# Optimization experiments

Hardware: AMD Instinct MI355X
Metric: run time of the kernel (lower is better)

Reference implementation:

```python
import jax, jax.numpy as jnp
import numpy as np

B, L = 2, 1024
D_MODEL, N_LAYER, VOCAB = 768, 4, 32000
D_INNER, D_STATE, D_CONV = 2 * D_MODEL, 16, 4
DT_RANK = (D_MODEL + 15) // 16  # 48


def setup_inputs() -> dict:
    key = jax.random.key(0)
    ks = jax.random.split(key, 8)
    s = 0.02
    nl = N_LAYER
    A_init = jnp.tile(jnp.log(jnp.arange(1.0, D_STATE + 1.0, dtype=jnp.float32))[None, None, :], (nl, D_INNER, 1))
    return {
        "sequence": jax.random.randint(ks[0], (B, L), 0, VOCAB),
        "sequence_mask": jnp.ones((B, L), dtype=jnp.int32),
        "emb": jax.random.normal(ks[1], (VOCAB, D_MODEL)) * s,
        "norm_w": jnp.ones((nl, D_MODEL)),
        "in_proj_w": jax.random.normal(ks[2], (nl, 2 * D_INNER, D_MODEL)) * s,
        "conv_w": jax.random.normal(ks[3], (nl, D_INNER, D_CONV)) * s,
        "conv_b": jnp.zeros((nl, D_INNER)),
        "x_proj_w": jax.random.normal(ks[4], (nl, DT_RANK + 2 * D_STATE, D_INNER)) * s,
        "dt_w": jax.random.normal(ks[5], (nl, D_INNER, DT_RANK)) * s,
        "dt_b": jnp.log(jnp.expm1(jnp.full((nl, D_INNER), 1e-2))),  # inv-softplus(dt_init)
        "A_log": A_init,
        "D_skip": jnp.ones((nl, D_INNER)),
        "out_w": jax.random.normal(ks[6], (nl, D_MODEL, D_INNER)) * s,
        "normf_w": jnp.ones((D_MODEL,)),
    }


def _rmsnorm(x, w, eps=1e-5):
    x = x.astype(jnp.float32)
    return x * jax.lax.rsqrt(jnp.mean(x * x, axis=-1, keepdims=True) + eps) * w


def _mamba_block(h, in_w, cw, cb, xpw, dtw, dtb, a_log, d_skip, ow):
    # h: [B, L, D_MODEL]
    Bsz, Lsz, _ = h.shape
    xz = jnp.einsum('bld,ed->ble', h, in_w)  # [B, L, 2*d_inner]
    x, z = jnp.split(xz, 2, axis=-1)
    # causal depthwise conv1d, kernel D_CONV
    xp = jnp.pad(x, ((0, 0), (D_CONV - 1, 0), (0, 0)))
    x = sum(xp[:, k:k + Lsz, :] * cw[:, k] for k in range(D_CONV)) + cb
    x = jax.nn.silu(x)
    xdbl = jnp.einsum('bld,ed->ble', x, xpw)  # [B, L, dt_rank + 2*d_state]
    dt = xdbl[..., :DT_RANK]
    Bm = xdbl[..., DT_RANK:DT_RANK + D_STATE]
    Cm = xdbl[..., DT_RANK + D_STATE:]
    delta = jax.nn.softplus(jnp.einsum('blr,dr->bld', dt, dtw) + dtb)  # [B, L, d_inner]
    A = -jnp.exp(a_log)  # [d_inner, d_state]

    def step(hstate, inp):
        d_t, b_t, c_t, u_t = inp  # [B,di],[B,ds],[B,ds],[B,di]
        dA = jnp.exp(d_t[..., None] * A)  # [B, di, ds]
        hstate = dA * hstate + (d_t * u_t)[..., None] * b_t[:, None, :]
        y = jnp.einsum('bds,bs->bd', hstate, c_t)
        return hstate, y

    h0 = jnp.zeros((Bsz, D_INNER, D_STATE), dtype=x.dtype)
    _, ys = jax.lax.scan(
        step, h0,
        (delta.transpose(1, 0, 2), Bm.transpose(1, 0, 2), Cm.transpose(1, 0, 2), x.transpose(1, 0, 2)))
    y = ys.transpose(1, 0, 2) + x * d_skip
    y = y * jax.nn.silu(z)
    return jnp.einsum('bld,ed->ble', y, ow)


def _forward(sequence, sequence_mask, emb, norm_w, in_proj_w, conv_w, conv_b,
             x_proj_w, dt_w, dt_b, A_log, D_skip, out_w, normf_w):
    residual = emb[sequence]  # [B, L, D]
    for i in range(norm_w.shape[0]):
        hn = _rmsnorm(residual, norm_w[i])
        residual = residual + _mamba_block(hn, in_proj_w[i], conv_w[i], conv_b[i],
                                           x_proj_w[i], dt_w[i], dt_b[i],
                                           A_log[i], D_skip[i], out_w[i])
    out = _rmsnorm(residual, normf_w)  # [B, L, D]
    last = sequence_mask.sum(-1).astype(jnp.int32) - 1
    return out[jnp.arange(out.shape[0]), last]  # [B, D] last valid hidden state


def reference(sequence, sequence_mask, emb, norm_w, in_proj_w, conv_w, conv_b,
              x_proj_w, dt_w, dt_b, A_log, D_skip, out_w, normf_w):
    return _forward(sequence, sequence_mask, emb, norm_w, in_proj_w, conv_w, conv_b,
                    x_proj_w, dt_w, dt_b, A_log, D_skip, out_w, normf_w)
```

## Files before the change

### kernel.cpp

```cpp
#include <hip/hip_runtime.h>
#include <hip/hip_bf16.h>

#define BSZ 2
#define LSEQ 1024
#define DMODEL 768
#define NLAYER 4
#define DINNER 1536
#define DSTATE 16
#define DCONV 4
#define DTRANK 48
#define NCHUNK 64
#define CLEN 16
#define XDSTR 128
#define XZLD (2 * DINNER)

typedef __bf16 bf16x8_t __attribute__((ext_vector_type(8)));
typedef float f32x4_t __attribute__((ext_vector_type(4)));
typedef unsigned short u16x8_t __attribute__((ext_vector_type(8)));
typedef __hip_bfloat16 bf16;

__device__ inline float bfbits2f(unsigned short u) {
    unsigned int x = ((unsigned int)u) << 16;
    return __builtin_bit_cast(float, x);
}
__device__ inline unsigned short f2bfbits(float f) {
    return __builtin_bit_cast(unsigned short, (__bf16)f);
}

__device__ __forceinline__ void gload16(const bf16* g, bf16* l) {
    __builtin_amdgcn_global_load_lds(
        (const __attribute__((address_space(1))) unsigned int*)g,
        (__attribute__((address_space(3))) unsigned int*)l,
        16, 0, 0);
}

__device__ inline float block_reduce_sum(float v, float* sbuf) {
    __syncthreads();
    #pragma unroll
    for (int o = 32; o > 0; o >>= 1) v += __shfl_down(v, o, 64);
    int wid = threadIdx.x >> 6;
    int lane = threadIdx.x & 63;
    if (lane == 0) sbuf[wid] = v;
    __syncthreads();
    if (threadIdx.x == 0) sbuf[0] = (sbuf[0] + sbuf[1]) + (sbuf[2] + sbuf[3]);
    __syncthreads();
    return sbuf[0];
}

#define PN1 (NLAYER * 3072 * 768)
#define PN2 (NLAYER * 768 * 1536)
#define PN3 (NLAYER * 128 * 1536)
#define PN4 (BSZ * LSEQ * DMODEL)
#define PN5 (2 * BSZ * LSEQ * XDSTR)
__global__ __launch_bounds__(256) void init_kernel(
    const int* __restrict__ seq, const float* __restrict__ emb,
    const float* __restrict__ in_w, const float* __restrict__ out_w,
    const float* __restrict__ xp_w,
    float* __restrict__ residual, bf16* __restrict__ in16,
    bf16* __restrict__ out16, bf16* __restrict__ xp16, float* __restrict__ xdbl2) {
    int idx = blockIdx.x * 256 + threadIdx.x;
    if (idx < PN1) { in16[idx] = __float2bfloat16(in_w[idx]); return; }
    idx -= PN1;
    if (idx < PN2) { out16[idx] = __float2bfloat16(out_w[idx]); return; }
    idx -= PN2;
    if (idx < PN3) {
        int l = idx / (128 * DINNER);
        int r = idx - l * (128 * DINNER);
        int e = r / DINNER;
        int k = r - e * DINNER;
        xp16[idx] = (e < 80) ? __float2bfloat16(xp_w[((size_t)l * 80 + e) * DINNER + k])
                             : __float2bfloat16(0.f);
        return;
    }
    idx -= PN3;
    if (idx < PN4) {
        int bl = idx / DMODEL;
        int dd = idx - bl * DMODEL;
        residual[idx] = emb[(size_t)seq[bl] * DMODEL + dd];
        return;
    }
    idx -= PN4;
    xdbl2[idx] = 0.f;
}

__global__ __launch_bounds__(256) void rmsnorm_kernel(
    const float* __restrict__ res, const float* __restrict__ w, bf16* __restrict__ out) {
    __shared__ float sbuf[8];
    int row = blockIdx.x;
    const float* x = res + (size_t)row * DMODEL;
    float ss = 0.f;
    for (int i = threadIdx.x; i < DMODEL; i += 256) { float v = x[i]; ss += v * v; }
    ss = block_reduce_sum(ss, sbuf);
    float scale = rsqrtf(ss / (float)DMODEL + 1e-5f);
    for (int i = threadIdx.x; i < DMODEL; i += 256)
        out[(size_t)row * DMODEL + i] = __float2bfloat16(x[i] * scale * w[i]);
}

__global__ __launch_bounds__(256) void rmsnorm_acc_kernel(
    float* __restrict__ res, const float* __restrict__ p0, const float* __restrict__ p1,
    const float* __restrict__ w, bf16* __restrict__ out) {
    __shared__ float sbuf[8];
    int row = blockIdx.x;
    size_t base = (size_t)row * DMODEL;
    float ss = 0.f;
    for (int i = threadIdx.x; i < DMODEL; i += 256) {
        float v = res[base + i] + p0[base + i] + p1[base + i];
        res[base + i] = v;
        ss += v * v;
    }
    ss = block_reduce_sum(ss, sbuf);
    float scale = rsqrtf(ss / (float)DMODEL + 1e-5f);
    for (int i = threadIdx.x; i < DMODEL; i += 256)
        out[base + i] = __float2bfloat16(res[base + i] * scale * w[i]);
}

__global__ __launch_bounds__(256) void gemm_128x64_g(
    const bf16* __restrict__ A, int lda, const bf16* __restrict__ Bw, int ldb,
    bf16* __restrict__ C16, int ldc, int K) {
    __shared__ bf16 As[128][64];
    __shared__ bf16 Bs[64][64];
    int tid = threadIdx.x;
    int wave = tid >> 6;
    int lane = tid & 63;
    int quad = lane >> 4;
    int l16 = lane & 15;
    int bm = blockIdx.x * 128;
    int bn = blockIdx.y * 64;
    int wm = wave * 32;
    int lr = lane >> 3;
    int lc = (lane & 7) ^ lr;
    int sx = (l16 & 7) << 3;

    f32x4_t acc[2][4];
    #pragma unroll
    for (int i = 0; i < 2; ++i)
        #pragma unroll
        for (int j = 0; j < 4; ++j) acc[i][j] = (f32x4_t){0.f, 0.f, 0.f, 0.f};

    for (int k0 = 0; k0 < K; k0 += 64) {
        #pragma unroll
        for (int i = 0; i < 6; ++i) {
            int ch = wave * 6 + i;
            if (ch < 16) {
                int r = ch * 8 + lr;
                gload16(A + (size_t)(bm + r) * lda + k0 + lc * 8, &As[ch * 8][0]);
            } else {
                int c2 = ch - 16;
                int r = c2 * 8 + lr;
                gload16(Bw + (size_t)(bn + r) * ldb + k0 + lc * 8, &Bs[c2 * 8][0]);
            }
        }
        __syncthreads();
        #pragma unroll
        for (int kk = 0; kk < 64; kk += 32) {
            bf16x8_t af[2], bf[4];
            #pragma unroll
            for (int i = 0; i < 2; ++i)
                af[i] = *(const bf16x8_t*)(&As[wm + i * 16 + l16][(kk + quad * 8) ^ sx]);
            #pragma unroll
            for (int j = 0; j < 4; ++j)
                bf[j] = *(const bf16x8_t*)(&Bs[j * 16 + l16][(kk + quad * 8) ^ sx]);
            #pragma unroll
            for (int i = 0; i < 2; ++i)
                #pragma unroll
                for (int j = 0; j < 4; ++j)
                    acc[i][j] = __builtin_amdgcn_mfma_f32_16x16x32_bf16(af[i], bf[j], acc[i][j], 0, 0, 0);
        }
        __syncthreads();
    }

    int mbase = bm + wm + quad * 4;
    #pragma unroll
    for (int i = 0; i < 2; ++i)
        #pragma unroll
        for (int j = 0; j < 4; ++j) {
            int n = bn + j * 16 + l16;
            #pragma unroll
            for (int r = 0; r < 4; ++r)
                C16[(size_t)(mbase + i * 16 + r) * ldc + n] = __float2bfloat16(acc[i][j][r]);
        }
}

__global__ __launch_bounds__(256) void gemm_64_atomic_g(
    const bf16* __restrict__ A, int lda, const bf16* __restrict__ Bw, int ldb,
    float* __restrict__ Cf, int ldc, int K) {
    __shared__ bf16 As[64][64];
    __shared__ bf16 Bs[64][64];
    int tid = threadIdx.x;
    int wave = tid >> 6;
    int lane = tid & 63;
    int quad = lane >> 4;
    int l16 = lane & 15;
    int bm = blockIdx.x * 64;
    int bn = blockIdx.y * 64;
    int lr = lane >> 3;
    int lc = (lane & 7) ^ lr;
    int sx = (l16 & 7) << 3;
    int kpb = K / gridDim.z;
    int kbeg = blockIdx.z * kpb;
    int kend = kbeg + kpb;

    f32x4_t acc[4];
    #pragma unroll
    for (int i = 0; i < 4; ++i) acc[i] = (f32x4_t){0.f, 0.f, 0.f, 0.f};

    for (int k0 = kbeg; k0 < kend; k0 += 64) {
        #pragma unroll
        for (int i = 0; i < 4; ++i) {
            int ch = wave * 4 + i;
            if (ch < 8) {
                int r = ch * 8 + lr;
                gload16(A + (size_t)(bm + r) * lda + k0 + lc * 8, &As[ch * 8][0]);
            } else {
                int c2 = ch - 8;
                int r = c2 * 8 + lr;
                gload16(Bw + (size_t)(bn + r) * ldb + k0 + lc * 8, &Bs[c2 * 8][0]);
            }
        }
        __syncthreads();
        #pragma unroll
        for (int kk = 0; kk < 64; kk += 32) {
            bf16x8_t af = *(const bf16x8_t*)(&As[wave * 16 + l16][(kk + quad * 8) ^ sx]);
            #pragma unroll
            for (int i = 0; i < 4; ++i) {
                bf16x8_t bv = *(const bf16x8_t*)(&Bs[i * 16 + l16][(kk + quad * 8) ^ sx]);
                acc[i] = __builtin_amdgcn_mfma_f32_16x16x32_bf16(af, bv, acc[i], 0, 0, 0);
            }
        }
        __syncthreads();
    }

    int m0 = bm + wave * 16 + quad * 4;
    #pragma unroll
    for (int i = 0; i < 4; ++i) {
        int n = bn + i * 16 + l16;
        #pragma unroll
        for (int r = 0; r < 4; ++r)
            atomicAdd(&Cf[(size_t)(m0 + r) * ldc + n], acc[i][r]);
    }
}

__global__ __launch_bounds__(256) void gemm_64_part_g(
    const bf16* __restrict__ A, int lda, const bf16* __restrict__ Bw, int ldb,
    float* __restrict__ P0, float* __restrict__ P1, int ldc, int K) {
    __shared__ bf16 As[64][64];
    __shared__ bf16 Bs[64][64];
    int tid = threadIdx.x;
    int wave = tid >> 6;
    int lane = tid & 63;
    int quad = lane >> 4;
    int l16 = lane & 15;
    int bm = blockIdx.x * 64;
    int bn = blockIdx.y * 64;
    int lr = lane >> 3;
    int lc = (lane & 7) ^ lr;
    int sx = (l16 & 7) << 3;
    int kpb = K / gridDim.z;
    int kbeg = blockIdx.z * kpb;
    int kend = kbeg + kpb;
    float* Cf = (blockIdx.z == 0) ? P0 : P1;

    f32x4_t acc[4];
    #pragma unroll
    for (int i = 0; i < 4; ++i) acc[i] = (f32x4_t){0.f, 0.f, 0.f, 0.f};

    for (int k0 = kbeg; k0 < kend; k0 += 64) {
        #pragma unroll
        for (int i = 0; i < 4; ++i) {
            int ch = wave * 4 + i;
            if (ch < 8) {
                int r = ch * 8 + lr;
                gload16(A + (size_t)(bm + r) * lda + k0 + lc * 8, &As[ch * 8][0]);
            } else {
                int c2 = ch - 8;
                int r = c2 * 8 + lr;
                gload16(Bw + (size_t)(bn + r) * ldb + k0 + lc * 8, &Bs[c2 * 8][0]);
            }
        }
        __syncthreads();
        #pragma unroll
        for (int kk = 0; kk < 64; kk += 32) {
            bf16x8_t af = *(const bf16x8_t*)(&As[wave * 16 + l16][(kk + quad * 8) ^ sx]);
            #pragma unroll
            for (int i = 0; i < 4; ++i) {
                bf16x8_t bv = *(const bf16x8_t*)(&Bs[i * 16 + l16][(kk + quad * 8) ^ sx]);
                acc[i] = __builtin_amdgcn_mfma_f32_16x16x32_bf16(af, bv, acc[i], 0, 0, 0);
            }
        }
        __syncthreads();
    }

    int m0 = bm + wave * 16 + quad * 4;
    #pragma unroll
    for (int i = 0; i < 4; ++i) {
        int n = bn + i * 16 + l16;
        #pragma unroll
        for (int r = 0; r < 4; ++r)
            Cf[(size_t)(m0 + r) * ldc + n] = acc[i][r];
    }
}

#define UCHUNKS (DINNER / 8)
__global__ __launch_bounds__(256) void usilu_kernel(
    const bf16* __restrict__ xz16, const float* __restrict__ cw, const float* __restrict__ cb,
    bf16* __restrict__ u16) {
    int idx = blockIdx.x * 256 + threadIdx.x;
    int row = idx / UCHUNKS;
    int d0 = (idx - row * UCHUNKS) * 8;
    int l = row & (LSEQ - 1);
    const u16x8_t Z8 = (u16x8_t){0, 0, 0, 0, 0, 0, 0, 0};
    u16x8_t xa[4];
    #pragma unroll
    for (int t = 0; t < 4; ++t)
        xa[t] = (l >= 3 - t) ? *(const u16x8_t*)(xz16 + (size_t)(row - 3 + t) * XZLD + d0) : Z8;
    u16x8_t r;
    #pragma unroll
    for (int j = 0; j < 8; ++j) {
        float4 cwv = *(const float4*)(cw + (size_t)(d0 + j) * 4);
        float a = cb[d0 + j]
            + bfbits2f(xa[0][j]) * cwv.x + bfbits2f(xa[1][j]) * cwv.y
            + bfbits2f(xa[2][j]) * cwv.z + bfbits2f(xa[3][j]) * cwv.w;
        a = a / (1.f + __expf(-a));
        r[j] = f2bfbits(a);
    }
    *(u16x8_t*)(u16 + (size_t)row * DINNER + d0) = r;
}

__device__ inline float compute_delta(const float* __restrict__ xrow,
                                      const float* __restrict__ dtw, float dtbd) {
    float acc = dtbd;
    #pragma unroll
    for (int j = 0; j < DTRANK; j += 4) {
        float4 xv = *(const float4*)(xrow + j);
        acc += xv.x * dtw[j] + xv.y * dtw[j + 1] + xv.z * dtw[j + 2] + xv.w * dtw[j + 3];
    }
    return (acc > 20.f) ? acc : log1pf(__expf(acc));
}

__global__ __launch_bounds__(256) void scan_phaseA(
    const bf16* __restrict__ u16, const float* __restrict__ xdbl,
    const float* __restrict__ dt_w, const float* __restrict__ dt_b,
    const float* __restrict__ A_log,
    float* __restrict__ Psum, float* __restrict__ Ssum,
    float* __restrict__ xd_next) {
    int gtid = blockIdx.x * 256 + threadIdx.x;
    int d = gtid % DINNER;
    int c = (gtid / DINNER) % NCHUNK;
    int b = gtid / (DINNER * NCHUNK);
    float dtw[DTRANK];
    #pragma unroll
    for (int j = 0; j < DTRANK; j += 4)
        *(float4*)(dtw + j) = *(const float4*)(dt_w + (size_t)d * DTRANK + j);
    float dtbd = dt_b[d];
    float Av[DSTATE], P[DSTATE], S[DSTATE];
    #pragma unroll
    for (int s = 0; s < DSTATE; ++s) {
        Av[s] = -__expf(A_log[d * DSTATE + s]);
        P[s] = 1.f; S[s] = 0.f;
    }
    int t0 = c * CLEN;
    int rowb = b * LSEQ;
    for (int i = 0; i < CLEN; ++i) {
        int row = rowb + t0 + i;
        const float* xrow = xdbl + (size_t)row * XDSTR;
        float dl = compute_delta(xrow, dtw, dtbd);
        float u = __bfloat162float(u16[(size_t)row * DINNER + d]);
        float bt = dl * u;
        const float4* Bp = (const float4*)(xrow + DTRANK);
        float4 B0 = Bp[0], B1 = Bp[1], B2 = Bp[2], B3 = Bp[3];
        float Bv[DSTATE] = {B0.x,B0.y,B0.z,B0.w, B1.x,B1.y,B1.z,B1.w,
                            B2.x,B2.y,B2.z,B2.w, B3.x,B3.y,B3.z,B3.w};
        #pragma unroll
        for (int s = 0; s < DSTATE; ++s) {
            float a = __expf(dl * Av[s]);
            P[s] *= a;
            S[s] = a * S[s] + bt * Bv[s];
        }
    }
    size_t base = ((size_t)(b * NCHUNK + c) * DSTATE) * DINNER + d;
    #pragma unroll
    for (int s = 0; s < DSTATE; ++s) {
        Psum[base + (size_t)s * DINNER] = P[s];
        Ssum[base + (size_t)s * DINNER] = S[s];
    }
    for (int z = gtid; z < BSZ * LSEQ * XDSTR; z += BSZ * NCHUNK * DINNER)
        xd_next[z] = 0.f;
}

__global__ __launch_bounds__(256) void scan_phaseB(
    const float* __restrict__ Psum, const float* __restrict__ Ssum,
    float* __restrict__ Hin) {
    int gtid = blockIdx.x * 256 + threadIdx.x;
    int d = gtid % DINNER;
    int s = (gtid / DINNER) % DSTATE;
    int b = gtid / (DINNER * DSTATE);
    float h = 0.f;
    for (int c = 0; c < NCHUNK; ++c) {
        size_t idx = ((size_t)(b * NCHUNK + c) * DSTATE + s) * DINNER + d;
        Hin[idx] = h;
        h = Psum[idx] * h + Ssum[idx];
    }
}

__global__ __launch_bounds__(256) void scan_phaseC(
    bf16* __restrict__ uy16, const bf16* __restrict__ xz16,
    const float* __restrict__ xdbl,
    const float* __restrict__ dt_w, const float* __restrict__ dt_b,
    const float* __restrict__ A_log, const float* __restrict__ D_skip,
    const float* __restrict__ Hin) {
    int gtid = blockIdx.x * 256 + threadIdx.x;
    int d = gtid % DINNER;
    int c = (gtid / DINNER) % NCHUNK;
    int b = gtid / (DINNER * NCHUNK);
    float dtw[DTRANK];
    #pragma unroll
    for (int j = 0; j < DTRANK; j += 4)
        *(float4*)(dtw + j) = *(const float4*)(dt_w + (size_t)d * DTRANK + j);
    float dtbd = dt_b[d];
    float Av[DSTATE], h[DSTATE];
    size_t base = ((size_t)(b * NCHUNK + c) * DSTATE) * DINNER + d;
    #pragma unroll
    for (int s = 0; s < DSTATE; ++s) {
        Av[s] = -__expf(A_log[d * DSTATE + s]);
        h[s] = Hin[base + (size_t)s * DINNER];
    }
    float Dsk = D_skip[d];
    int t0 = c * CLEN;
    int rowb = b * LSEQ;
    for (int i = 0; i < CLEN; ++i) {
        int row = rowb + t0 + i;
        const float* xrow = xdbl + (size_t)row * XDSTR;
        float dl = compute_delta(xrow, dtw, dtbd);
        float u = __bfloat162float(uy16[(size_t)row * DINNER + d]);
        float bt = dl * u;
        const float4* Bp = (const float4*)(xrow + DTRANK);
        float4 B0 = Bp[0], B1 = Bp[1], B2 = Bp[2], B3 = Bp[3];
        const float4* Cp = (const float4*)(xrow + DTRANK + DSTATE);
        float4 C0 = Cp[0], C1 = Cp[1], C2 = Cp[2], C3 = Cp[3];
        float Bv[DSTATE] = {B0.x,B0.y,B0.z,B0.w, B1.x,B1.y,B1.z,B1.w,
                            B2.x,B2.y,B2.z,B2.w, B3.x,B3.y,B3.z,B3.w};
        float Cv[DSTATE] = {C0.x,C0.y,C0.z,C0.w, C1.x,C1.y,C1.z,C1.w,
                            C2.x,C2.y,C2.z,C2.w, C3.x,C3.y,C3.z,C3.w};
        float acc = 0.f;
        #pragma unroll
        for (int s = 0; s < DSTATE; ++s) {
            float a = __expf(dl * Av[s]);
            h[s] = a * h[s] + bt * Bv[s];
            acc += h[s] * Cv[s];
        }
        float zv = __bfloat162float(xz16[(size_t)row * XZLD + DINNER + d]);
        float sz = zv / (1.f + __expf(-zv));
        uy16[(size_t)row * DINNER + d] = __float2bfloat16((acc + u * Dsk) * sz);
    }
}

__global__ __launch_bounds__(256) void final_acc_kernel(
    const float* __restrict__ res, const float* __restrict__ p0, const float* __restrict__ p1,
    const int* __restrict__ mask, const float* __restrict__ w, float* __restrict__ out) {
    __shared__ float sbuf[8];
    int b = blockIdx.x;
    float cnt = 0.f;
    for (int i = threadIdx.x; i < LSEQ; i += 256) cnt += (float)mask[b * LSEQ + i];
    cnt = block_reduce_sum(cnt, sbuf);
    int last = (int)cnt - 1;
    size_t base = ((size_t)b * LSEQ + last) * DMODEL;
    float ss = 0.f;
    for (int i = threadIdx.x; i < DMODEL; i += 256) {
        float v = res[base + i] + p0[base + i] + p1[base + i];
        ss += v * v;
    }
    ss = block_reduce_sum(ss, sbuf);
    float scale = rsqrtf(ss / (float)DMODEL + 1e-5f);
    for (int i = threadIdx.x; i < DMODEL; i += 256) {
        float v = res[base + i] + p0[base + i] + p1[base + i];
        out[b * DMODEL + i] = v * scale * w[i];
    }
}

extern "C" void kernel_launch(void* const* d_in, const int* in_sizes, int n_in,
                              void* d_out, int out_size, void* d_ws, size_t ws_size,
                              hipStream_t stream) {
    const int*   seq      = (const int*)d_in[0];
    const int*   mask     = (const int*)d_in[1];
    const float* emb      = (const float*)d_in[2];
    const float* norm_w   = (const float*)d_in[3];
    const float* in_w     = (const float*)d_in[4];
    const float* conv_w   = (const float*)d_in[5];
    const float* conv_b   = (const float*)d_in[6];
    const float* xp_w     = (const float*)d_in[7];
    const float* dt_w     = (const float*)d_in[8];
    const float* dt_b     = (const float*)d_in[9];
    const float* A_log    = (const float*)d_in[10];
    const float* D_skip   = (const float*)d_in[11];
    const float* out_w    = (const float*)d_in[12];
    const float* normf_w  = (const float*)d_in[13];
    float* out = (float*)d_out;

    char* ws = (char*)d_ws;
    float* residual = (float*)(ws);
    bf16*  hn16     = (bf16*)(ws + 6291456);
    bf16*  xz16     = (bf16*)(ws + 9437184);
    float* xdbl     = (float*)(ws + 22020096);
    bf16*  uy16     = (bf16*)(ws + 24117248);
    float* Psum     = (float*)(ws + 30408704);
    float* Ssum     = (float*)(ws + 42991616);
    float* Hin      = (float*)(ws + 55574528);
    bf16*  in16     = (bf16*)(ws + 68157440);
    bf16*  out16    = (bf16*)(ws + 87031808);
    bf16*  xp16     = (bf16*)(ws + 96468992);
    float* P0 = Psum;
    float* P1 = Ssum;

    init_kernel<<<66560, 256, 0, stream>>>(seq, emb, in_w, out_w, xp_w,
                                           residual, in16, out16, xp16, xdbl);

    for (int i = 0; i < NLAYER; ++i) {
        float* xd_cur = xdbl + (size_t)(i & 1) * (BSZ * LSEQ * XDSTR);
        float* xd_nxt = xdbl + (size_t)((i + 1) & 1) * (BSZ * LSEQ * XDSTR);
        const float* cw = conv_w + (size_t)i * DINNER * DCONV;
        const float* cb = conv_b + (size_t)i * DINNER;
        const float* dw = dt_w + (size_t)i * DINNER * DTRANK;
        const float* db = dt_b + (size_t)i * DINNER;
        const float* al = A_log + (size_t)i * DINNER * DSTATE;

        if (i == 0)
            rmsnorm_kernel<<<BSZ * LSEQ, 256, 0, stream>>>(
                residual, norm_w, hn16);
        else
            rmsnorm_acc_kernel<<<BSZ * LSEQ, 256, 0, stream>>>(
                residual, P0, P1, norm_w + (size_t)i * DMODEL, hn16);
        gemm_128x64_g<<<dim3(16, 48), 256, 0, stream>>>(
            hn16, DMODEL, in16 + (size_t)i * 3072 * DMODEL, DMODEL, xz16, XZLD, DMODEL);
        usilu_kernel<<<(BSZ * LSEQ * UCHUNKS) / 256, 256, 0, stream>>>(xz16, cw, cb, uy16);
        gemm_64_atomic_g<<<dim3(32, 2, 8), 256, 0, stream>>>(
            uy16, DINNER, xp16 + (size_t)i * 128 * DINNER, DINNER, xd_cur, XDSTR, DINNER);
        scan_phaseA<<<768, 256, 0, stream>>>(
            uy16, xd_cur, dw, db, al, Psum, Ssum, xd_nxt);
        scan_phaseB<<<192, 256, 0, stream>>>(Psum, Ssum, Hin);
        scan_phaseC<<<768, 256, 0, stream>>>(
            uy16, xz16, xd_cur, dw, db, al, D_skip + (size_t)i * DINNER, Hin);
        gemm_64_part_g<<<dim3(32, 12, 2), 256, 0, stream>>>(
            uy16, DINNER, out16 + (size_t)i * DMODEL * DINNER, DINNER, P0, P1, DMODEL, DINNER);
    }

    final_acc_kernel<<<BSZ, 256, 0, stream>>>(residual, P0, P1, mask, normf_w, out);
}
```

Before: 791.2 us.

## Cache delta between scan phases and retile out_proj GEMM with 4-way split-K

Phase A now writes the softplus delta to a buffer, so phase C reads it back instead of recomputing the 48-wide dot product. Phase B overwrites Psum in place with each chunk's starting state, which removes the separate Hin buffer. The output projection moves to 128x64 tiles with four K-splits written to four partial buffers, and the rmsnorm and final kernels sum all four. This trades recompute and small tiles for extra memory traffic: a 12MB delta buffer plus twice as many partial-sum reads.

```diff
diff --git a/kernel.cpp b/kernel.cpp
--- a/kernel.cpp
+++ b/kernel.cpp
@@ -98,13 +98,14 @@
 
 __global__ __launch_bounds__(256) void rmsnorm_acc_kernel(
     float* __restrict__ res, const float* __restrict__ p0, const float* __restrict__ p1,
+    const float* __restrict__ p2, const float* __restrict__ p3,
     const float* __restrict__ w, bf16* __restrict__ out) {
     __shared__ float sbuf[8];
     int row = blockIdx.x;
     size_t base = (size_t)row * DMODEL;
     float ss = 0.f;
     for (int i = threadIdx.x; i < DMODEL; i += 256) {
-        float v = res[base + i] + p0[base + i] + p1[base + i];
+        float v = res[base + i] + ((p0[base + i] + p1[base + i]) + (p2[base + i] + p3[base + i]));
         res[base + i] = v;
         ss += v * v;
     }
@@ -240,39 +241,43 @@
     }
 }
 
-__global__ __launch_bounds__(256) void gemm_64_part_g(
+__global__ __launch_bounds__(256) void gemm_128x64_part_g(
     const bf16* __restrict__ A, int lda, const bf16* __restrict__ Bw, int ldb,
-    float* __restrict__ P0, float* __restrict__ P1, int ldc, int K) {
-    __shared__ bf16 As[64][64];
+    float* __restrict__ P0, float* __restrict__ P1,
+    float* __restrict__ P2, float* __restrict__ P3, int ldc, int K) {
+    __shared__ bf16 As[128][64];
     __shared__ bf16 Bs[64][64];
     int tid = threadIdx.x;
     int wave = tid >> 6;
     int lane = tid & 63;
     int quad = lane >> 4;
     int l16 = lane & 15;
-    int bm = blockIdx.x * 64;
+    int bm = blockIdx.x * 128;
     int bn = blockIdx.y * 64;
+    int wm = wave * 32;
     int lr = lane >> 3;
     int lc = (lane & 7) ^ lr;
     int sx = (l16 & 7) << 3;
-    int kpb = K / gridDim.z;
+    int kpb = K / 4;
     int kbeg = blockIdx.z * kpb;
     int kend = kbeg + kpb;
-    float* Cf = (blockIdx.z == 0) ? P0 : P1;
-
-    f32x4_t acc[4];
-    #pragma unroll
-    for (int i = 0; i < 4; ++i) acc[i] = (f32x4_t){0.f, 0.f, 0.f, 0.f};
+    float* Cf = (blockIdx.z == 0) ? P0 : (blockIdx.z == 1) ? P1 : (blockIdx.z == 2) ? P2 : P3;
+
+    f32x4_t acc[2][4];
+    #pragma unroll
+    for (int i = 0; i < 2; ++i)
+        #pragma unroll
+        for (int j = 0; j < 4; ++j) acc[i][j] = (f32x4_t){0.f, 0.f, 0.f, 0.f};
 
     for (int k0 = kbeg; k0 < kend; k0 += 64) {
         #pragma unroll
-        for (int i = 0; i < 4; ++i) {
-            int ch = wave * 4 + i;
-            if (ch < 8) {
+        for (int i = 0; i < 6; ++i) {
+            int ch = wave * 6 + i;
+            if (ch < 16) {
                 int r = ch * 8 + lr;
                 gload16(A + (size_t)(bm + r) * lda + k0 + lc * 8, &As[ch * 8][0]);
             } else {
-                int c2 = ch - 8;
+                int c2 = ch - 16;
                 int r = c2 * 8 + lr;
                 gload16(Bw + (size_t)(bn + r) * ldb + k0 + lc * 8, &Bs[c2 * 8][0]);
             }
@@ -280,24 +285,32 @@
         __syncthreads();
         #pragma unroll
         for (int kk = 0; kk < 64; kk += 32) {
-            bf16x8_t af = *(const bf16x8_t*)(&As[wave * 16 + l16][(kk + quad * 8) ^ sx]);
-            #pragma unroll
-            for (int i = 0; i < 4; ++i) {
-                bf16x8_t bv = *(const bf16x8_t*)(&Bs[i * 16 + l16][(kk + quad * 8) ^ sx]);
-                acc[i] = __builtin_amdgcn_mfma_f32_16x16x32_bf16(af, bv, acc[i], 0, 0, 0);
-            }
+            bf16x8_t af[2], bf[4];
+            #pragma unroll
+            for (int i = 0; i < 2; ++i)
+                af[i] = *(const bf16x8_t*)(&As[wm + i * 16 + l16][(kk + quad * 8) ^ sx]);
+            #pragma unroll
+            for (int j = 0; j < 4; ++j)
+                bf[j] = *(const bf16x8_t*)(&Bs[j * 16 + l16][(kk + quad * 8) ^ sx]);
+            #pragma unroll
+            for (int i = 0; i < 2; ++i)
+                #pragma unroll
+                for (int j = 0; j < 4; ++j)
+                    acc[i][j] = __builtin_amdgcn_mfma_f32_16x16x32_bf16(af[i], bf[j], acc[i][j], 0, 0, 0);
         }
         __syncthreads();
     }
 
-    int m0 = bm + wave * 16 + quad * 4;
-    #pragma unroll
-    for (int i = 0; i < 4; ++i) {
-        int n = bn + i * 16 + l16;
-        #pragma unroll
-        for (int r = 0; r < 4; ++r)
-            Cf[(size_t)(m0 + r) * ldc + n] = acc[i][r];
-    }
+    int mbase = bm + wm + quad * 4;
+    #pragma unroll
+    for (int i = 0; i < 2; ++i)
+        #pragma unroll
+        for (int j = 0; j < 4; ++j) {
+            int n = bn + j * 16 + l16;
+            #pragma unroll
+            for (int r = 0; r < 4; ++r)
+                Cf[(size_t)(mbase + i * 16 + r) * ldc + n] = acc[i][j][r];
+        }
 }
 
 #define UCHUNKS (DINNER / 8)
@@ -342,6 +355,7 @@
     const float* __restrict__ dt_w, const float* __restrict__ dt_b,
     const float* __restrict__ A_log,
     float* __restrict__ Psum, float* __restrict__ Ssum,
+    float* __restrict__ Dbuf,
     float* __restrict__ xd_next) {
     int gtid = blockIdx.x * 256 + threadIdx.x;
     int d = gtid % DINNER;
@@ -364,6 +378,7 @@
         int row = rowb + t0 + i;
         const float* xrow = xdbl + (size_t)row * XDSTR;
         float dl = compute_delta(xrow, dtw, dtbd);
+        Dbuf[(size_t)row * DINNER + d] = dl;
         float u = __bfloat162float(u16[(size_t)row * DINNER + d]);
         float bt = dl * u;
         const float4* Bp = (const float4*)(xrow + DTRANK);
@@ -388,8 +403,7 @@
 }
 
 __global__ __launch_bounds__(256) void scan_phaseB(
-    const float* __restrict__ Psum, const float* __restrict__ Ssum,
-    float* __restrict__ Hin) {
+    float* __restrict__ Psum, const float* __restrict__ Ssum) {
     int gtid = blockIdx.x * 256 + threadIdx.x;
     int d = gtid % DINNER;
     int s = (gtid / DINNER) % DSTATE;
@@ -397,32 +411,27 @@
     float h = 0.f;
     for (int c = 0; c < NCHUNK; ++c) {
         size_t idx = ((size_t)(b * NCHUNK + c) * DSTATE + s) * DINNER + d;
-        Hin[idx] = h;
-        h = Psum[idx] * h + Ssum[idx];
+        float p = Psum[idx];
+        Psum[idx] = h;
+        h = p * h + Ssum[idx];
     }
 }
 
 __global__ __launch_bounds__(256) void scan_phaseC(
     bf16* __restrict__ uy16, const bf16* __restrict__ xz16,
     const float* __restrict__ xdbl,
-    const float* __restrict__ dt_w, const float* __restrict__ dt_b,
     const float* __restrict__ A_log, const float* __restrict__ D_skip,
-    const float* __restrict__ Hin) {
+    const float* __restrict__ H0, const float* __restrict__ Dbuf) {
     int gtid = blockIdx.x * 256 + threadIdx.x;
     int d = gtid % DINNER;
     int c = (gtid / DINNER) % NCHUNK;
     int b = gtid / (DINNER * NCHUNK);
-    float dtw[DTRANK];
-    #pragma unroll
-    for (int j = 0; j < DTRANK; j += 4)
-        *(float4*)(dtw + j) = *(const float4*)(dt_w + (size_t)d * DTRANK + j);
-    float dtbd = dt_b[d];
     float Av[DSTATE], h[DSTATE];
     size_t base = ((size_t)(b * NCHUNK + c) * DSTATE) * DINNER + d;
     #pragma unroll
     for (int s = 0; s < DSTATE; ++s) {
         Av[s] = -__expf(A_log[d * DSTATE + s]);
-        h[s] = Hin[base + (size_t)s * DINNER];
+        h[s] = H0[base + (size_t)s * DINNER];
     }
     float Dsk = D_skip[d];
     int t0 = c * CLEN;
@@ -430,7 +439,7 @@
     for (int i = 0; i < CLEN; ++i) {
         int row = rowb + t0 + i;
         const float* xrow = xdbl + (size_t)row * XDSTR;
-        float dl = compute_delta(xrow, dtw, dtbd);
+        float dl = Dbuf[(size_t)row * DINNER + d];
         float u = __bfloat162float(uy16[(size_t)row * DINNER + d]);
         float bt = dl * u;
         const float4* Bp = (const float4*)(xrow + DTRANK);
@@ -456,6 +465,7 @@
 
 __global__ __launch_bounds__(256) void final_acc_kernel(
     const float* __restrict__ res, const float* __restrict__ p0, const float* __restrict__ p1,
+    const float* __restrict__ p2, const float* __restrict__ p3,
     const int* __restrict__ mask, const float* __restrict__ w, float* __restrict__ out) {
     __shared__ float sbuf[8];
     int b = blockIdx.x;
@@ -466,13 +476,13 @@
     size_t base = ((size_t)b * LSEQ + last) * DMODEL;
     float ss = 0.f;
     for (int i = threadIdx.x; i < DMODEL; i += 256) {
-        float v = res[base + i] + p0[base + i] + p1[base + i];
+        float v = res[base + i] + ((p0[base + i] + p1[base + i]) + (p2[base + i] + p3[base + i]));
         ss += v * v;
     }
     ss = block_reduce_sum(ss, sbuf);
     float scale = rsqrtf(ss / (float)DMODEL + 1e-5f);
     for (int i = threadIdx.x; i < DMODEL; i += 256) {
-        float v = res[base + i] + p0[base + i] + p1[base + i];
+        float v = res[base + i] + ((p0[base + i] + p1[base + i]) + (p2[base + i] + p3[base + i]));
         out[b * DMODEL + i] = v * scale * w[i];
     }
 }
@@ -504,12 +514,14 @@
     bf16*  uy16     = (bf16*)(ws + 24117248);
     float* Psum     = (float*)(ws + 30408704);
     float* Ssum     = (float*)(ws + 42991616);
-    float* Hin      = (float*)(ws + 55574528);
+    float* Dbuf     = (float*)(ws + 55574528);
     bf16*  in16     = (bf16*)(ws + 68157440);
     bf16*  out16    = (bf16*)(ws + 87031808);
     bf16*  xp16     = (bf16*)(ws + 96468992);
     float* P0 = Psum;
-    float* P1 = Ssum;
+    float* P1 = Psum + (size_t)BSZ * LSEQ * DMODEL;
+    float* P2 = Ssum;
+    float* P3 = Ssum + (size_t)BSZ * LSEQ * DMODEL;
 
     init_kernel<<<66560, 256, 0, stream>>>(seq, emb, in_w, out_w, xp_w,
                                            residual, in16, out16, xp16, xdbl);
@@ -528,20 +540,21 @@
                 residual, norm_w, hn16);
         else
             rmsnorm_acc_kernel<<<BSZ * LSEQ, 256, 0, stream>>>(
-                residual, P0, P1, norm_w + (size_t)i * DMODEL, hn16);
+                residual, P0, P1, P2, P3, norm_w + (size_t)i * DMODEL, hn16);
         gemm_128x64_g<<<dim3(16, 48), 256, 0, stream>>>(
             hn16, DMODEL, in16 + (size_t)i * 3072 * DMODEL, DMODEL, xz16, XZLD, DMODEL);
         usilu_kernel<<<(BSZ * LSEQ * UCHUNKS) / 256, 256, 0, stream>>>(xz16, cw, cb, uy16);
         gemm_64_atomic_g<<<dim3(32, 2, 8), 256, 0, stream>>>(
             uy16, DINNER, xp16 + (size_t)i * 128 * DINNER, DINNER, xd_cur, XDSTR, DINNER);
         scan_phaseA<<<768, 256, 0, stream>>>(
-            uy16, xd_cur, dw, db, al, Psum, Ssum, xd_nxt);
-        scan_phaseB<<<192, 256, 0, stream>>>(Psum, Ssum, Hin);
+            uy16, xd_cur, dw, db, al, Psum, Ssum, Dbuf, xd_nxt);
+        scan_phaseB<<<192, 256, 0, stream>>>(Psum, Ssum);
         scan_phaseC<<<768, 256, 0, stream>>>(
-            uy16, xz16, xd_cur, dw, db, al, D_skip + (size_t)i * DINNER, Hin);
-        gemm_64_part_g<<<dim3(32, 12, 2), 256, 0, stream>>>(
-            uy16, DINNER, out16 + (size_t)i * DMODEL * DINNER, DINNER, P0, P1, DMODEL, DINNER);
-    }
-
-    final_acc_kernel<<<BSZ, 256, 0, stream>>>(residual, P0, P1, mask, normf_w, out);
-}
+            uy16, xz16, xd_cur, al, D_skip + (size_t)i * DINNER, Psum, Dbuf);
+        gemm_128x64_part_g<<<dim3(16, 12, 4), 256, 0, stream>>>(
+            uy16, DINNER, out16 + (size_t)i * DMODEL * DINNER, DINNER,
+            P0, P1, P2, P3, DMODEL, DINNER);
+    }
+
+    final_acc_kernel<<<BSZ, 256, 0, stream>>>(residual, P0, P1, P2, P3, mask, normf_w, out);
+}
```

New measurement: 702.7 us. 11.2% less time.
